# Kernel optimization log

Measured on AMD Instinct MI355X. Metric: run time of the kernel, lower is better.

## Reference

```python
import jax, jax.numpy as jnp
import numpy as np

HID = 1024       # hidden_size
H = 8            # num_attention_heads
KVH = 2          # num_key_value_heads
D = HID // H     # head_dim = 128
WINDOW = 2048    # sliding_window
THETA = 10000.0  # rope_theta
B, S = 1, 4096


def rotate_half(x):
    x1, x2 = jnp.split(x, 2, axis=-1)
    return jnp.concatenate([-x2, x1], axis=-1)


def setup_inputs() -> dict:
    key = jax.random.key(0)
    ks = jax.random.split(key, 5)
    scale = 0.02
    return {
        "hidden_states": jax.random.normal(ks[0], (B, S, HID), dtype=jnp.float32),
        "wq": jax.random.normal(ks[1], (H * D, HID), dtype=jnp.float32) * scale,
        "wk": jax.random.normal(ks[2], (KVH * D, HID), dtype=jnp.float32) * scale,
        "wv": jax.random.normal(ks[3], (KVH * D, HID), dtype=jnp.float32) * scale,
        "wo": jax.random.normal(ks[4], (HID, H * D), dtype=jnp.float32) * scale,
        "position_ids": jnp.broadcast_to(jnp.arange(S, dtype=jnp.int64 if jax.config.jax_enable_x64 else jnp.int32)[None, :], (B, S)),
    }


def reference(hidden_states, wq, wk, wv, wo, position_ids):
    b, s, _ = hidden_states.shape
    # projections (torch nn.Linear: x @ W^T)
    q = (hidden_states @ wq.T).reshape(b, s, H, D).transpose(0, 2, 1, 3)      # bhsd
    k = (hidden_states @ wk.T).reshape(b, s, KVH, D).transpose(0, 2, 1, 3)    # b(kv)sd
    v = (hidden_states @ wv.T).reshape(b, s, KVH, D).transpose(0, 2, 1, 3)

    # RoPE cache (head_dim, seq_len)
    inv_freq = 1.0 / THETA ** (jnp.arange(0, D, 2, dtype=jnp.float32) / D)
    t = jnp.arange(s, dtype=jnp.float32)
    freqs = t[:, None] * inv_freq[None, :]
    emb = jnp.concatenate([freqs, freqs], axis=-1)           # (S, D)
    cos = jnp.cos(emb)[position_ids][:, None]                # (B,1,S,D)
    sin = jnp.sin(emb)[position_ids][:, None]
    q = q * cos + rotate_half(q) * sin
    k = k * cos + rotate_half(k) * sin

    # GQA: repeat kv heads to match query heads (repeat_interleave on head dim)
    groups = H // KVH
    k = jnp.repeat(k, groups, axis=1)
    v = jnp.repeat(v, groups, axis=1)

    # full score matrix with sliding-window causal mask
    scores = jnp.einsum("bhqd,bhkd->bhqk", q, k)
    i = jnp.arange(s)[:, None]
    j = jnp.arange(s)[None, :]
    mask = (j <= i) & (j > i - WINDOW)                       # causal + window
    scores = jnp.where(mask[None, None], scores, -jnp.inf) / jnp.sqrt(jnp.float32(D))

    probs = jax.nn.softmax(scores.astype(jnp.float32), axis=-1).astype(q.dtype)
    ctx = jnp.einsum("bhqk,bhkd->bhqd", probs, v)
    ctx = ctx.transpose(0, 2, 1, 3).reshape(b, s, H * D)
    return ctx @ wo.T
```

## Files before the change

kernel.cpp:

```cpp
#include <hip/hip_runtime.h>

#define S_LEN 4096
#define HIDDEN 1024
#define NH 8
#define NKV 2
#define HD 128
#define WIN 2048

typedef short bf16x8 __attribute__((ext_vector_type(8)));
typedef short bf16x4 __attribute__((ext_vector_type(4)));
typedef float f32x4 __attribute__((ext_vector_type(4)));
typedef unsigned short u16x4 __attribute__((ext_vector_type(4)));

__device__ __forceinline__ unsigned short f2b(float f) {
    unsigned int u = __builtin_bit_cast(unsigned int, f);
    u += 0x7fffu + ((u >> 16) & 1u);
    return (unsigned short)(u >> 16);
}
__device__ __forceinline__ float b2f(unsigned short u) {
    unsigned int x = ((unsigned int)u) << 16;
    return __builtin_bit_cast(float, x);
}

__device__ __forceinline__ void gl_lds16(const unsigned short* g, unsigned short* l) {
    __builtin_amdgcn_global_load_lds(
        (const __attribute__((address_space(1))) unsigned int*)g,
        (__attribute__((address_space(3))) unsigned int*)l, 16, 0, 0);
}

#define WAIT_VM4   0x0F74
#define WAIT_VM0   0x0F70
#define WAIT_LGKM0 0xC07F
#define MEMFENCE() __asm__ volatile("" ::: "memory")

__global__ __launch_bounds__(256) void cvt5(
    const float* __restrict__ s0, unsigned short* __restrict__ t0, int n0,
    const float* __restrict__ s1, unsigned short* __restrict__ t1, int n1,
    const float* __restrict__ s2, unsigned short* __restrict__ t2, int n2,
    const float* __restrict__ s3, unsigned short* __restrict__ t3, int n3,
    const float* __restrict__ s4, unsigned short* __restrict__ t4, int n4)
{
    int i = blockIdx.x * 256 + threadIdx.x;
    const float* s; unsigned short* t;
    if (i < n0)              { s = s0; t = t0; }
    else if ((i -= n0) < n1) { s = s1; t = t1; }
    else if ((i -= n1) < n2) { s = s2; t = t2; }
    else if ((i -= n2) < n3) { s = s3; t = t3; }
    else if ((i -= n3) < n4) { s = s4; t = t4; }
    else return;
    f32x4 v = *(const f32x4*)(s + (size_t)i * 4);
    u16x4 r = { f2b(v[0]), f2b(v[1]), f2b(v[2]), f2b(v[3]) };
    *(u16x4*)(t + (size_t)i * 4) = r;
}

__global__ __launch_bounds__(256, 2) void gemm128(
    const unsigned short* __restrict__ A, const unsigned short* __restrict__ W,
    float* __restrict__ Cf, unsigned short* __restrict__ Cb,
    int M, int N, int K)
{
    __shared__ alignas(16) unsigned short As[3][128 * 32];
    __shared__ alignas(16) unsigned short Bs[3][128 * 32];

    int lane = threadIdx.x & 63;
    int w = threadIdx.x >> 6;
    int l15 = lane & 15, quad = lane >> 4;

    int tiles_n = N >> 7;
    int mt0 = (int)blockIdx.x / tiles_n;
    int nt0 = (int)blockIdx.x - mt0 * tiles_n;

    size_t goffA[2], goffB[2];
    #pragma unroll
    for (int is = 0; is < 2; ++is) {
        int s = w * 128 + is * 64 + lane;
        int row = s >> 2, spos = s & 3;
        int kblk = spos ^ ((row >> 1) & 3);
        goffA[is] = (size_t)(mt0 * 128 + row) * K + kblk * 8;
        goffB[is] = (size_t)(nt0 * 128 + row) * K + kblk * 8;
    }

    int arow0 = (w >> 1) * 64;
    int brow0 = (w & 1) * 64;
    int aoff[4], boff[4];
    #pragma unroll
    for (int t = 0; t < 4; ++t) {
        int ra = arow0 + t * 16 + l15;
        aoff[t] = (ra * 4 + (quad ^ ((ra >> 1) & 3))) * 8;
        int rb = brow0 + t * 16 + l15;
        boff[t] = (rb * 4 + (quad ^ ((rb >> 1) & 3))) * 8;
    }

    f32x4 acc[4][4];
    #pragma unroll
    for (int i = 0; i < 4; ++i)
        #pragma unroll
        for (int j = 0; j < 4; ++j) acc[i][j] = (f32x4){0.f, 0.f, 0.f, 0.f};

    auto stage = [&](int i) {
        int b = i % 3, k0 = i * 32;
        gl_lds16(A + goffA[0] + k0, &As[b][(w * 128 + 0) * 8]);
        gl_lds16(A + goffA[1] + k0, &As[b][(w * 128 + 64) * 8]);
        gl_lds16(W + goffB[0] + k0, &Bs[b][(w * 128 + 0) * 8]);
        gl_lds16(W + goffB[1] + k0, &Bs[b][(w * 128 + 64) * 8]);
    };

    int nk = K >> 5;
    stage(0);
    if (nk > 1) stage(1);
    for (int i = 0; i < nk; ++i) {
        MEMFENCE();
        if (i + 1 < nk) __builtin_amdgcn_s_waitcnt(WAIT_VM4);
        else            __builtin_amdgcn_s_waitcnt(WAIT_VM0);
        __builtin_amdgcn_s_barrier();
        MEMFENCE();
        if (i + 2 < nk) stage(i + 2);

        const unsigned short* Ab = &As[i % 3][0];
        const unsigned short* Bb = &Bs[i % 3][0];
        bf16x8 af[4], bf_[4];
        #pragma unroll
        for (int t = 0; t < 4; ++t) {
            af[t]  = *(const bf16x8*)(Ab + aoff[t]);
            bf_[t] = *(const bf16x8*)(Bb + boff[t]);
        }
        #pragma unroll
        for (int i2 = 0; i2 < 4; ++i2)
            #pragma unroll
            for (int j = 0; j < 4; ++j)
                acc[i2][j] = __builtin_amdgcn_mfma_f32_16x16x32_bf16(af[i2], bf_[j], acc[i2][j], 0, 0, 0);
        MEMFENCE();
    }

    #pragma unroll
    for (int i = 0; i < 4; ++i) {
        int row0 = mt0 * 128 + arow0 + i * 16 + quad * 4;
        #pragma unroll
        for (int j = 0; j < 4; ++j) {
            int col = nt0 * 128 + brow0 + j * 16 + l15;
            if (Cf) {
                #pragma unroll
                for (int reg = 0; reg < 4; ++reg)
                    Cf[(size_t)(row0 + reg) * N + col] = acc[i][j][reg];
            } else {
                #pragma unroll
                for (int reg = 0; reg < 4; ++reg)
                    Cb[(size_t)(row0 + reg) * N + col] = f2b(acc[i][j][reg]);
            }
        }
    }
}

#define QKVW (HIDDEN + 2 * NKV * HD)
__global__ __launch_bounds__(256, 2) void gemmqkv(
    const unsigned short* __restrict__ A, const unsigned short* __restrict__ W,
    const int* __restrict__ pos,
    unsigned short* __restrict__ Qb, unsigned short* __restrict__ Kb,
    unsigned short* __restrict__ Vt)
{
    __shared__ alignas(16) char pool[49152];
    unsigned short (*As)[128 * 32] = (unsigned short (*)[128 * 32])(pool);
    unsigned short (*Bs)[128 * 32] = (unsigned short (*)[128 * 32])(pool + 24576);
    float (*Ex)[32][68] = (float (*)[32][68])(pool);
    unsigned short* T = (unsigned short*)(pool);

    int lane = threadIdx.x & 63;
    int w = threadIdx.x >> 6;
    int l15 = lane & 15, quad = lane >> 4;

    const int K = HIDDEN;
    int mt0 = (int)blockIdx.x / 12;
    int nt0 = (int)blockIdx.x - mt0 * 12;

    size_t goffA[2], goffB[2];
    #pragma unroll
    for (int is = 0; is < 2; ++is) {
        int s = w * 128 + is * 64 + lane;
        int row = s >> 2, spos = s & 3;
        int kblk = spos ^ ((row >> 1) & 3);
        goffA[is] = (size_t)(mt0 * 128 + row) * K + kblk * 8;
        goffB[is] = (size_t)(nt0 * 128 + row) * K + kblk * 8;
    }

    int arow0 = (w >> 1) * 64;
    int brow0 = (w & 1) * 64;
    int aoff[4], boff[4];
    #pragma unroll
    for (int t = 0; t < 4; ++t) {
        int ra = arow0 + t * 16 + l15;
        aoff[t] = (ra * 4 + (quad ^ ((ra >> 1) & 3))) * 8;
        int rb = brow0 + t * 16 + l15;
        boff[t] = (rb * 4 + (quad ^ ((rb >> 1) & 3))) * 8;
    }

    f32x4 acc[4][4];
    #pragma unroll
    for (int i = 0; i < 4; ++i)
        #pragma unroll
        for (int j = 0; j < 4; ++j) acc[i][j] = (f32x4){0.f, 0.f, 0.f, 0.f};

    auto stage = [&](int i) {
        int b = i % 3, k0 = i * 32;
        gl_lds16(A + goffA[0] + k0, &As[b][(w * 128 + 0) * 8]);
        gl_lds16(A + goffA[1] + k0, &As[b][(w * 128 + 64) * 8]);
        gl_lds16(W + goffB[0] + k0, &Bs[b][(w * 128 + 0) * 8]);
        gl_lds16(W + goffB[1] + k0, &Bs[b][(w * 128 + 64) * 8]);
    };

    stage(0);
    stage(1);
    for (int i = 0; i < 32; ++i) {
        MEMFENCE();
        if (i + 1 < 32) __builtin_amdgcn_s_waitcnt(WAIT_VM4);
        else            __builtin_amdgcn_s_waitcnt(WAIT_VM0);
        __builtin_amdgcn_s_barrier();
        MEMFENCE();
        if (i + 2 < 32) stage(i + 2);

        const unsigned short* Ab = &As[i % 3][0];
        const unsigned short* Bb = &Bs[i % 3][0];
        bf16x8 af[4], bf_[4];
        #pragma unroll
        for (int t = 0; t < 4; ++t) {
            af[t]  = *(const bf16x8*)(Ab + aoff[t]);
            bf_[t] = *(const bf16x8*)(Bb + boff[t]);
        }
        #pragma unroll
        for (int i2 = 0; i2 < 4; ++i2)
            #pragma unroll
            for (int j = 0; j < 4; ++j)
                acc[i2][j] = __builtin_amdgcn_mfma_f32_16x16x32_bf16(af[i2], bf_[j], acc[i2][j], 0, 0, 0);
        MEMFENCE();
    }

    if (nt0 >= 10) {
        int kv = nt0 - 10;
        __syncthreads();
        #pragma unroll
        for (int i = 0; i < 4; ++i) {
            int srow = arow0 + i * 16 + quad * 4;
            #pragma unroll
            for (int j = 0; j < 4; ++j) {
                int d = brow0 + j * 16 + l15;
                #pragma unroll
                for (int reg = 0; reg < 4; ++reg)
                    T[(srow + reg) * 130 + d] = f2b(acc[i][j][reg]);
            }
        }
        __syncthreads();
        int tid = threadIdx.x;
        int dl = tid >> 5;
        int sc4 = (tid & 31) * 4;
        #pragma unroll
        for (int it = 0; it < 16; ++it) {
            int d = it * 8 + dl;
            u16x4 v4 = { T[(sc4 + 0) * 130 + d], T[(sc4 + 1) * 130 + d],
                         T[(sc4 + 2) * 130 + d], T[(sc4 + 3) * 130 + d] };
            *(u16x4*)(Vt + (size_t)kv * HD * S_LEN + (size_t)d * S_LEN
                      + mt0 * 128 + sc4) = v4;
        }
        return;
    }

    bool isQ = (nt0 < 8);
    int kv = nt0 - 8;
    bool is64 = (pos[1] == 0) && (pos[3] == 0);
    const float qscale = 0.08838834764831843f;

    float invf[4];
    #pragma unroll
    for (int j = 0; j < 4; ++j) {
        int d6 = (brow0 + j * 16 + l15) & 63;
        invf[j] = exp2f(-(float)d6 * (13.287712379549449f / 64.0f));
    }

    #pragma unroll
    for (int r2 = 0; r2 < 2; ++r2) {
        __syncthreads();
        #pragma unroll
        for (int ii = 0; ii < 2; ++ii) {
            int i = r2 * 2 + ii;
            #pragma unroll
            for (int j = 0; j < 4; ++j)
                #pragma unroll
                for (int reg = 0; reg < 4; ++reg)
                    Ex[w][ii * 16 + quad * 4 + reg][j * 16 + l15] = acc[i][j][reg];
        }
        __syncthreads();
        #pragma unroll
        for (int ii = 0; ii < 2; ++ii) {
            int i = r2 * 2 + ii;
            #pragma unroll
            for (int reg = 0; reg < 4; ++reg) {
                int s = mt0 * 128 + arow0 + i * 16 + quad * 4 + reg;
                int pv_ = is64 ? pos[2 * s] : pos[s];
                float pf = (float)pv_;
                #pragma unroll
                for (int j = 0; j < 4; ++j) {
                    float sn, cs;
                    __sincosf(pf * invf[j], &sn, &cs);
                    float a  = acc[i][j][reg];
                    float pr = Ex[w ^ 1][ii * 16 + quad * 4 + reg][j * 16 + l15];
                    int d_local = brow0 + j * 16 + l15;
                    float outv = (d_local < 64) ? (a * cs - pr * sn) : (a * cs + pr * sn);
                    if (isQ) {
                        Qb[(size_t)s * HIDDEN + nt0 * HD + d_local] = f2b(outv * qscale);
                    } else {
                        Kb[(size_t)kv * S_LEN * HD + (size_t)s * HD + d_local] = f2b(outv);
                    }
                }
            }
        }
    }
}

__global__ __launch_bounds__(256, 2) void attn_coop(
    const unsigned short* __restrict__ Qb, const unsigned short* __restrict__ Kb,
    const unsigned short* __restrict__ Vt, unsigned short* __restrict__ Ctx)
{
    __shared__ alignas(16) unsigned short Klds[2][64 * 128];
    __shared__ alignas(16) unsigned short Vlds[2][128 * 64];

    int lane = threadIdx.x & 63;
    int w = threadIdx.x >> 6;
    int l15 = lane & 15, quad = lane >> 4;
    int h = blockIdx.y;
    int kv = h >> 2;
    int qt = (h & 4) ? (63 - (int)blockIdx.x) : (int)blockIdx.x;
    int qb = qt * 64;
    int q16 = qb + w * 16;

    bf16x8 a_q[4];
    const unsigned short* qrow = Qb + (size_t)(q16 + l15) * HIDDEN + h * HD + quad * 8;
    #pragma unroll
    for (int st = 0; st < 4; ++st) a_q[st] = *(const bf16x8*)(qrow + st * 32);

    bf16x4 ones4;
    #pragma unroll
    for (int i = 0; i < 4; ++i) ones4[i] = (short)0x3F80;

    int lo = qb + 63 - (WIN - 1); if (lo < 0) lo = 0; lo &= ~63;
    int nch = (qb + 64 - lo) >> 6;

    const unsigned short* gbase;
    unsigned short* ldsdst[2];
    int myoff[8];
    int jmul;
    if (w < 2) {
        gbase = Kb + (size_t)kv * S_LEN * HD;
        ldsdst[0] = &Klds[0][w * 8 * 512];
        ldsdst[1] = &Klds[1][w * 8 * 512];
        jmul = HD;
        #pragma unroll
        for (int tt = 0; tt < 8; ++tt) {
            int t = w * 8 + tt;
            int key  = t * 4 + (lane >> 4);
            int dblk = (lane & 15) ^ (key & 15);
            myoff[tt] = key * HD + dblk * 8;
        }
    } else {
        gbase = Vt + (size_t)kv * HD * S_LEN;
        ldsdst[0] = &Vlds[0][(w - 2) * 8 * 512];
        ldsdst[1] = &Vlds[1][(w - 2) * 8 * 512];
        jmul = 1;
        #pragma unroll
        for (int tt = 0; tt < 8; ++tt) {
            int t = (w - 2) * 8 + tt;
            int d    = t * 8 + (lane >> 3);
            int kblk = (lane & 7) ^ (d & 7);
            myoff[tt] = d * S_LEN + kblk * 8;
        }
    }

    auto issue = [&](int c) {
        int j0 = lo + c * 64;
        const unsigned short* src = gbase + (size_t)j0 * jmul;
        unsigned short* dst = ldsdst[c & 1];
        #pragma unroll
        for (int tt = 0; tt < 8; ++tt)
            gl_lds16(src + myoff[tt], dst + tt * 512);
    };

    f32x4 o[9];
    #pragma unroll
    for (int nd = 0; nd < 9; ++nd) o[nd] = (f32x4){0.f, 0.f, 0.f, 0.f};

    issue(0);

    for (int c = 0; c < nch; ++c) {
        int j0 = lo + c * 64;

        MEMFENCE();
        __builtin_amdgcn_s_waitcnt(WAIT_VM0);
        __builtin_amdgcn_s_barrier();
        MEMFENCE();
        if (c + 1 < nch) issue(c + 1);

        const unsigned short* Kc = &Klds[c & 1][0];
        const unsigned short* Vc = &Vlds[c & 1][0];

        f32x4 sc[4];
        #pragma unroll
        for (int t = 0; t < 4; ++t) {
            sc[t] = (f32x4){0.f, 0.f, 0.f, 0.f};
            int key = t * 16 + l15;
            #pragma unroll
            for (int st = 0; st < 4; ++st) {
                int off16 = key * 16 + ((st * 4 + quad) ^ (key & 15));
                bf16x8 ak = *(const bf16x8*)(Kc + off16 * 8);
                sc[t] = __builtin_amdgcn_mfma_f32_16x16x32_bf16(ak, a_q[st], sc[t], 0, 0, 0);
            }
        }

        float p[4][4];
        if (j0 + 63 <= q16 && j0 > q16 + 15 - WIN) {
            #pragma unroll
            for (int t = 0; t < 4; ++t)
                #pragma unroll
                for (int reg = 0; reg < 4; ++reg) p[t][reg] = __expf(sc[t][reg]);
        } else {
            int iq = q16 + l15;
            #pragma unroll
            for (int t = 0; t < 4; ++t) {
                #pragma unroll
                for (int reg = 0; reg < 4; ++reg) {
                    int key = j0 + t * 16 + quad * 4 + reg;
                    p[t][reg] = (key <= iq && key > iq - WIN) ? __expf(sc[t][reg]) : 0.f;
                }
            }
        }

        bf16x4 a_p[4];
        #pragma unroll
        for (int t = 0; t < 4; ++t) {
            a_p[t][0] = (short)f2b(p[t][0]);
            a_p[t][1] = (short)f2b(p[t][1]);
            a_p[t][2] = (short)f2b(p[t][2]);
            a_p[t][3] = (short)f2b(p[t][3]);
        }

        #pragma unroll
        for (int t = 0; t < 4; ++t) {
            #pragma unroll
            for (int nd = 0; nd < 8; ++nd) {
                int d = nd * 16 + l15;
                int kblk = t * 2 + (quad >> 1);
                int slot = d * 8 + (kblk ^ (d & 7));
                bf16x4 bv = *(const bf16x4*)(Vc + slot * 8 + (quad & 1) * 4);
                o[nd] = __builtin_amdgcn_mfma_f32_16x16x16bf16_1k(a_p[t], bv, o[nd], 0, 0, 0);
            }
            o[8] = __builtin_amdgcn_mfma_f32_16x16x16bf16_1k(a_p[t], ones4, o[8], 0, 0, 0);
        }
        MEMFENCE();
    }

    #pragma unroll
    for (int nd = 0; nd < 8; ++nd) {
        int d = nd * 16 + l15;
        #pragma unroll
        for (int reg = 0; reg < 4; ++reg) {
            int q = q16 + quad * 4 + reg;
            Ctx[(size_t)q * HIDDEN + h * HD + d] = f2b(o[nd][reg] / o[8][reg]);
        }
    }
}

extern "C" void kernel_launch(void* const* d_in, const int* in_sizes, int n_in,
                              void* d_out, int out_size, void* d_ws, size_t ws_size,
                              hipStream_t stream)
{
    const float* hidden = (const float*)d_in[0];
    const float* wq = (const float*)d_in[1];
    const float* wk = (const float*)d_in[2];
    const float* wv = (const float*)d_in[3];
    const float* wo = (const float*)d_in[4];
    const int* pos = (const int*)d_in[5];
    float* out = (float*)d_out;

    char* ws = (char*)d_ws;
    size_t off = 0;
    unsigned short* Hb   = (unsigned short*)(ws + off); off += (size_t)S_LEN * HIDDEN * 2;
    unsigned short* Wqkv = (unsigned short*)(ws + off); off += (size_t)QKVW * HIDDEN * 2;
    unsigned short* Wob  = (unsigned short*)(ws + off); off += (size_t)HIDDEN * HIDDEN * 2;
    unsigned short* Qb   = (unsigned short*)(ws + off); off += (size_t)S_LEN * HIDDEN * 2;
    unsigned short* Kb   = (unsigned short*)(ws + off); off += (size_t)S_LEN * NKV * HD * 2;
    unsigned short* Vt   = (unsigned short*)(ws + off); off += (size_t)S_LEN * NKV * HD * 2;
    unsigned short* Cb   = (unsigned short*)(ws + off); off += (size_t)S_LEN * HIDDEN * 2;

    const int n_h  = S_LEN * HIDDEN / 4;
    const int n_wq = HIDDEN * HIDDEN / 4;
    const int n_wk = NKV * HD * HIDDEN / 4;
    int tot4 = n_h + n_wq + 2 * n_wk + n_wq;
    cvt5<<<(tot4 + 255) / 256, 256, 0, stream>>>(
        hidden, Hb, n_h,
        wq, Wqkv, n_wq,
        wk, Wqkv + (size_t)HIDDEN * HIDDEN, n_wk,
        wv, Wqkv + (size_t)(HIDDEN + NKV * HD) * HIDDEN, n_wk,
        wo, Wob, n_wq);

    gemmqkv<<<(S_LEN / 128) * 12, 256, 0, stream>>>(
        Hb, Wqkv, pos, Qb, Kb, Vt);

    attn_coop<<<dim3(S_LEN / 64, NH), 256, 0, stream>>>(Qb, Kb, Vt, Cb);

    gemm128<<<(S_LEN / 128) * (HIDDEN / 128), 256, 0, stream>>>(
        Cb, Wob, out, nullptr, S_LEN, HIDDEN, HIDDEN);
}
```

Measured before the change: 187.3 us.

## Process 128 queries per attention block to reuse K/V tiles across two groups

Each wave now handles two 16-row query groups, so a block covers 128 queries and each K/V chunk loaded into LDS feeds twice as many MFMAs. This halves the grid and the total K/V traffic per head, and drops the reversed block ordering for the upper heads. In exchange register pressure roughly doubles (launch bounds no longer request 2 blocks per CU), occupancy falls, and the grid is only 256 blocks, which may underfill the GPU.

```diff
diff --git a/kernel.cpp b/kernel.cpp
--- a/kernel.cpp
+++ b/kernel.cpp
@@ -313,7 +313,7 @@
     }
 }
 
-__global__ __launch_bounds__(256, 2) void attn_coop(
+__global__ __launch_bounds__(256) void attn_coop(
     const unsigned short* __restrict__ Qb, const unsigned short* __restrict__ Kb,
     const unsigned short* __restrict__ Vt, unsigned short* __restrict__ Ctx)
 {
@@ -325,21 +325,24 @@
     int l15 = lane & 15, quad = lane >> 4;
     int h = blockIdx.y;
     int kv = h >> 2;
-    int qt = (h & 4) ? (63 - (int)blockIdx.x) : (int)blockIdx.x;
-    int qb = qt * 64;
-    int q16 = qb + w * 16;
-
-    bf16x8 a_q[4];
-    const unsigned short* qrow = Qb + (size_t)(q16 + l15) * HIDDEN + h * HD + quad * 8;
-    #pragma unroll
-    for (int st = 0; st < 4; ++st) a_q[st] = *(const bf16x8*)(qrow + st * 32);
+    int qb = blockIdx.x * 128;
+    int q16g[2] = { qb + w * 32, qb + w * 32 + 16 };
+
+    bf16x8 a_q[2][4];
+    #pragma unroll
+    for (int g = 0; g < 2; ++g) {
+        const unsigned short* qrow =
+            Qb + (size_t)(q16g[g] + l15) * HIDDEN + h * HD + quad * 8;
+        #pragma unroll
+        for (int st = 0; st < 4; ++st) a_q[g][st] = *(const bf16x8*)(qrow + st * 32);
+    }
 
     bf16x4 ones4;
     #pragma unroll
     for (int i = 0; i < 4; ++i) ones4[i] = (short)0x3F80;
 
-    int lo = qb + 63 - (WIN - 1); if (lo < 0) lo = 0; lo &= ~63;
-    int nch = (qb + 64 - lo) >> 6;
+    int lo = qb - (WIN - 1); if (lo < 0) lo = 0; lo &= ~63;
+    int nch = (qb + 128 - lo) >> 6;
 
     const unsigned short* gbase;
     unsigned short* ldsdst[2];
@@ -380,9 +383,11 @@
             gl_lds16(src + myoff[tt], dst + tt * 512);
     };
 
-    f32x4 o[9];
-    #pragma unroll
-    for (int nd = 0; nd < 9; ++nd) o[nd] = (f32x4){0.f, 0.f, 0.f, 0.f};
+    f32x4 o[2][9];
+    #pragma unroll
+    for (int g = 0; g < 2; ++g)
+        #pragma unroll
+        for (int nd = 0; nd < 9; ++nd) o[g][nd] = (f32x4){0.f, 0.f, 0.f, 0.f};
 
     issue(0);
 
@@ -398,44 +403,43 @@
         const unsigned short* Kc = &Klds[c & 1][0];
         const unsigned short* Vc = &Vlds[c & 1][0];
 
-        f32x4 sc[4];
+        f32x4 sc[2][4];
         #pragma unroll
         for (int t = 0; t < 4; ++t) {
-            sc[t] = (f32x4){0.f, 0.f, 0.f, 0.f};
+            sc[0][t] = (f32x4){0.f, 0.f, 0.f, 0.f};
+            sc[1][t] = (f32x4){0.f, 0.f, 0.f, 0.f};
             int key = t * 16 + l15;
             #pragma unroll
             for (int st = 0; st < 4; ++st) {
                 int off16 = key * 16 + ((st * 4 + quad) ^ (key & 15));
                 bf16x8 ak = *(const bf16x8*)(Kc + off16 * 8);
-                sc[t] = __builtin_amdgcn_mfma_f32_16x16x32_bf16(ak, a_q[st], sc[t], 0, 0, 0);
-            }
-        }
-
-        float p[4][4];
-        if (j0 + 63 <= q16 && j0 > q16 + 15 - WIN) {
-            #pragma unroll
-            for (int t = 0; t < 4; ++t)
-                #pragma unroll
-                for (int reg = 0; reg < 4; ++reg) p[t][reg] = __expf(sc[t][reg]);
-        } else {
-            int iq = q16 + l15;
-            #pragma unroll
-            for (int t = 0; t < 4; ++t) {
-                #pragma unroll
-                for (int reg = 0; reg < 4; ++reg) {
-                    int key = j0 + t * 16 + quad * 4 + reg;
-                    p[t][reg] = (key <= iq && key > iq - WIN) ? __expf(sc[t][reg]) : 0.f;
+                sc[0][t] = __builtin_amdgcn_mfma_f32_16x16x32_bf16(ak, a_q[0][st], sc[0][t], 0, 0, 0);
+                sc[1][t] = __builtin_amdgcn_mfma_f32_16x16x32_bf16(ak, a_q[1][st], sc[1][t], 0, 0, 0);
+            }
+        }
+
+        bf16x4 a_p[2][4];
+        #pragma unroll
+        for (int g = 0; g < 2; ++g) {
+            int q16 = q16g[g];
+            if (j0 + 63 <= q16 && j0 > q16 + 15 - WIN) {
+                #pragma unroll
+                for (int t = 0; t < 4; ++t)
+                    #pragma unroll
+                    for (int reg = 0; reg < 4; ++reg)
+                        a_p[g][t][reg] = (short)f2b(__expf(sc[g][t][reg]));
+            } else {
+                int iq = q16 + l15;
+                #pragma unroll
+                for (int t = 0; t < 4; ++t) {
+                    #pragma unroll
+                    for (int reg = 0; reg < 4; ++reg) {
+                        int key = j0 + t * 16 + quad * 4 + reg;
+                        float pv = (key <= iq && key > iq - WIN) ? __expf(sc[g][t][reg]) : 0.f;
+                        a_p[g][t][reg] = (short)f2b(pv);
+                    }
                 }
             }
-        }
-
-        bf16x4 a_p[4];
-        #pragma unroll
-        for (int t = 0; t < 4; ++t) {
-            a_p[t][0] = (short)f2b(p[t][0]);
-            a_p[t][1] = (short)f2b(p[t][1]);
-            a_p[t][2] = (short)f2b(p[t][2]);
-            a_p[t][3] = (short)f2b(p[t][3]);
         }
 
         #pragma unroll
@@ -446,22 +450,26 @@
                 int kblk = t * 2 + (quad >> 1);
                 int slot = d * 8 + (kblk ^ (d & 7));
                 bf16x4 bv = *(const bf16x4*)(Vc + slot * 8 + (quad & 1) * 4);
-                o[nd] = __builtin_amdgcn_mfma_f32_16x16x16bf16_1k(a_p[t], bv, o[nd], 0, 0, 0);
-            }
-            o[8] = __builtin_amdgcn_mfma_f32_16x16x16bf16_1k(a_p[t], ones4, o[8], 0, 0, 0);
-        }
-        MEMFENCE();
-    }
-
-    #pragma unroll
-    for (int nd = 0; nd < 8; ++nd) {
-        int d = nd * 16 + l15;
-        #pragma unroll
-        for (int reg = 0; reg < 4; ++reg) {
-            int q = q16 + quad * 4 + reg;
-            Ctx[(size_t)q * HIDDEN + h * HD + d] = f2b(o[nd][reg] / o[8][reg]);
-        }
-    }
+                o[0][nd] = __builtin_amdgcn_mfma_f32_16x16x16bf16_1k(a_p[0][t], bv, o[0][nd], 0, 0, 0);
+                o[1][nd] = __builtin_amdgcn_mfma_f32_16x16x16bf16_1k(a_p[1][t], bv, o[1][nd], 0, 0, 0);
+            }
+            o[0][8] = __builtin_amdgcn_mfma_f32_16x16x16bf16_1k(a_p[0][t], ones4, o[0][8], 0, 0, 0);
+            o[1][8] = __builtin_amdgcn_mfma_f32_16x16x16bf16_1k(a_p[1][t], ones4, o[1][8], 0, 0, 0);
+        }
+        MEMFENCE();
+    }
+
+    #pragma unroll
+    for (int g = 0; g < 2; ++g)
+        #pragma unroll
+        for (int nd = 0; nd < 8; ++nd) {
+            int d = nd * 16 + l15;
+            #pragma unroll
+            for (int reg = 0; reg < 4; ++reg) {
+                int q = q16g[g] + quad * 4 + reg;
+                Ctx[(size_t)q * HIDDEN + h * HD + d] = f2b(o[g][nd][reg] / o[g][8][reg]);
+            }
+        }
 }
 
 extern "C" void kernel_launch(void* const* d_in, const int* in_sizes, int n_in,
@@ -500,7 +508,7 @@
     gemmqkv<<<(S_LEN / 128) * 12, 256, 0, stream>>>(
         Hb, Wqkv, pos, Qb, Kb, Vt);
 
-    attn_coop<<<dim3(S_LEN / 64, NH), 256, 0, stream>>>(Qb, Kb, Vt, Cb);
+    attn_coop<<<dim3(S_LEN / 128, NH), 256, 0, stream>>>(Qb, Kb, Vt, Cb);
 
     gemm128<<<(S_LEN / 128) * (HIDDEN / 128), 256, 0, stream>>>(
         Cb, Wob, out, nullptr, S_LEN, HIDDEN, HIDDEN);
```

Measured after the change: 202.0 us. +7.9%, slower.
